# Optimization experiments

Hardware: AMD Instinct MI355X
Metric: run time of the kernel (lower is better)

Reference implementation:

```python
import jax, jax.numpy as jnp
import numpy as np

N_NODES = 65536   # sli * node = 512 * 128
N_EDGES = 524288  # avg degree 8
SLI, NODE = 512, 128
SLOPE = 0.01      # nn.LeakyReLU default negative_slope


def leaky_relu(v):
    return jnp.where(v >= 0, v, SLOPE * v)


def graph_conv(h, src, dst, W, b):
    """DGL GraphConv with norm='both': D_in^{-1/2} A D_out^{-1/2} h W + b, then LeakyReLU."""
    ones = jnp.ones(src.shape[0], dtype=h.dtype)
    out_deg = jnp.clip(jax.ops.segment_sum(ones, src, num_segments=N_NODES), 1.0)
    in_deg = jnp.clip(jax.ops.segment_sum(ones, dst, num_segments=N_NODES), 1.0)
    h = h * jax.lax.rsqrt(out_deg)[:, None]                     # src-side norm
    agg = jax.ops.segment_sum(h[src], dst, num_segments=N_NODES)  # gather + scatter-add
    agg = agg * jax.lax.rsqrt(in_deg)[:, None]                  # dst-side norm
    return leaky_relu(agg @ W + b)


def graphsage(x, src, dst, W, b):
    # x: [sli, C, node] -> [sli*node, C] -> GraphConv -> [sli, F, node]
    sli, C, node = x.shape
    h = x.transpose(0, 2, 1).reshape(-1, C)
    h = graph_conv(h, src, dst, W, b)
    return h.reshape(sli, node, -1).transpose(0, 2, 1)


def conv1x1(x, W, b):
    # pointwise Conv1d: x [S, Cin, N], W [Cout, Cin] -> [S, Cout, N]
    return jnp.einsum('scn,oc->son', x, W) + b[None, :, None]


def setup_inputs() -> dict:
    key = jax.random.key(0)
    ks = jax.random.split(key, 16)
    d = {
        'x': jax.random.normal(ks[0], (SLI, 128, NODE), dtype=jnp.float32),
        'edge_src': jax.random.randint(ks[1], (N_EDGES,), 0, N_NODES, dtype=jnp.int32),
        'edge_dst': jax.random.randint(ks[2], (N_EDGES,), 0, N_NODES, dtype=jnp.int32),
        'W_head': jax.random.normal(ks[3], (128, 128), dtype=jnp.float32) * 0.05,
        'b_head': jnp.zeros((128,), dtype=jnp.float32),
        'W_res0': jax.random.normal(ks[4], (128, 128), dtype=jnp.float32) * 0.05,
        'b_res0': jnp.zeros((128,), dtype=jnp.float32),
        'W_res1': jax.random.normal(ks[5], (128, 128), dtype=jnp.float32) * 0.05,
        'b_res1': jnp.zeros((128,), dtype=jnp.float32),
        'W_res2': jax.random.normal(ks[6], (128, 128), dtype=jnp.float32) * 0.05,
        'b_res2': jnp.zeros((128,), dtype=jnp.float32),
        'W_fusion': jax.random.normal(ks[7], (256, 512), dtype=jnp.float32) * 0.05,
        'b_fusion': jnp.zeros((256,), dtype=jnp.float32),
        'W_p1': jax.random.normal(ks[8], (256, 768), dtype=jnp.float32) * 0.05,
        'b_p1': jnp.zeros((256,), dtype=jnp.float32),
        'W_p2': jax.random.normal(ks[9], (64, 256), dtype=jnp.float32) * 0.05,
        'b_p2': jnp.zeros((64,), dtype=jnp.float32),
        'W_p3': jax.random.normal(ks[10], (2, 64), dtype=jnp.float32) * 0.05,
        'b_p3': jnp.zeros((2,), dtype=jnp.float32),
    }
    return d


def reference(x, edge_src, edge_dst, W_head, b_head, W_res0, b_res0, W_res1, b_res1,
              W_res2, b_res2, W_fusion, b_fusion, W_p1, b_p1, W_p2, b_p2, W_p3, b_p3):
    h = graphsage(x, edge_src, edge_dst, W_head, b_head)   # [S, 128, N]
    states = [h]
    for W, b in ((W_res0, b_res0), (W_res1, b_res1), (W_res2, b_res2)):
        h = graphsage(h, edge_src, edge_dst, W, b) + h     # residual
        states.append(h)
    state = jnp.concatenate(states, axis=1)                # [S, 512, N]
    fused = conv1x1(state, W_fusion, b_fusion)             # [S, 256, N]
    global_state = jnp.max(fused, axis=2, keepdims=True)   # [S, 256, 1]
    global_state = jnp.broadcast_to(global_state, (state.shape[0], 256, state.shape[2]))
    state = jnp.concatenate([global_state, state], axis=1) # [S, 768, N]
    y = leaky_relu(conv1x1(state, W_p1, b_p1))
    y = leaky_relu(conv1x1(y, W_p2, b_p2))
    return conv1x1(y, W_p3, b_p3)                          # [S, 2, N]
```

## Files before the change

### kernel.cpp

```cpp
#include <hip/hip_runtime.h>

#define NN 65536
#define NE 524288
#define SLOPE 0.01f

typedef unsigned short us;
typedef __attribute__((ext_vector_type(8))) short short8;
typedef __attribute__((ext_vector_type(4))) float f32x4;

__device__ __forceinline__ float leaky(float v) { return v >= 0.f ? v : SLOPE * v; }
__device__ __forceinline__ float b2f(us u) { return __uint_as_float(((unsigned)u) << 16); }
__device__ __forceinline__ us f2b(float f) {
  unsigned u = __float_as_uint(f);
  u += 0x7fffu + ((u >> 16) & 1u);
  return (us)(u >> 16);
}
__device__ __forceinline__ void split2(float v, us& hi, us& lo) {
  hi = f2b(v);
  lo = f2b(v - b2f(hi));
}

__device__ __forceinline__ void gload16(const void* g, void* l) {
  __builtin_amdgcn_global_load_lds(
      (const __attribute__((address_space(1))) unsigned int*)g,
      (__attribute__((address_space(3))) unsigned int*)l, 16, 0, 0);
}

__global__ void zero_ints(int* __restrict__ p, int n) {
  int i = blockIdx.x * blockDim.x + threadIdx.x;
  if (i < n) p[i] = 0;
}

__global__ void deg_count(const int* __restrict__ src, const int* __restrict__ dst,
                          int* __restrict__ cout, int* __restrict__ cin) {
  int e = blockIdx.x * blockDim.x + threadIdx.x;
  if (e < NE) {
    atomicAdd(&cout[src[e]], 1);
    atomicAdd(&cin[dst[e]], 1);
  }
}

__global__ void rs_kernel(const int* __restrict__ cout, const int* __restrict__ cin,
                          float* __restrict__ rs_out, float* __restrict__ rs_in) {
  int n = blockIdx.x * blockDim.x + threadIdx.x;
  if (n < NN) {
    rs_out[n] = rsqrtf((float)(cout[n] > 0 ? cout[n] : 1));
    rs_in[n]  = rsqrtf((float)(cin[n]  > 0 ? cin[n]  : 1));
  }
}

__global__ __launch_bounds__(1024) void scan_kernel(const int* __restrict__ cnt,
                                                    int* __restrict__ row_ptr) {
  __shared__ int part[1024];
  int t = threadIdx.x;
  int base = t * 64;
  int s = 0;
  for (int i = 0; i < 64; ++i) s += cnt[base + i];
  part[t] = s;
  __syncthreads();
  for (int d = 1; d < 1024; d <<= 1) {
    int v = (t >= d) ? part[t - d] : 0;
    __syncthreads();
    part[t] += v;
    __syncthreads();
  }
  int run = part[t] - s;
  for (int i = 0; i < 64; ++i) { row_ptr[base + i] = run; run += cnt[base + i]; }
  if (t == 1023) row_ptr[NN] = run;
}

__global__ void csr_fill(const int* __restrict__ src, const int* __restrict__ dst,
                         const int* __restrict__ row_ptr, int* __restrict__ cursor,
                         int* __restrict__ csr) {
  int e = blockIdx.x * blockDim.x + threadIdx.x;
  if (e < NE) {
    int d = dst[e];
    int pos = atomicAdd(&cursor[d], 1);
    csr[row_ptr[d] + pos] = src[e];
  }
}

__global__ __launch_bounds__(256) void transpose_x(const float* __restrict__ x,
                                                   us* __restrict__ h0h,
                                                   us* __restrict__ h0l) {
  __shared__ float tile[128][68];
  int s  = blockIdx.x >> 1;
  int vh = (blockIdx.x & 1) * 64;
  const float* xs = x + (size_t)s * 16384;
  int t = threadIdx.x;
  int v4 = t & 15, c0 = t >> 4;
  for (int p = 0; p < 8; ++p) {
    int c = c0 + p * 16;
    float4 val = *(const float4*)(xs + (size_t)c * 128 + vh + v4 * 4);
    *(float4*)&tile[c][v4 * 4] = val;
  }
  __syncthreads();
  int c4 = t & 31, v0 = t >> 5;
  for (int p = 0; p < 8; ++p) {
    int v = v0 + p * 8;
    float o[4];
    o[0] = tile[c4 * 4 + 0][v];
    o[1] = tile[c4 * 4 + 1][v];
    o[2] = tile[c4 * 4 + 2][v];
    o[3] = tile[c4 * 4 + 3][v];
    us hh[4], ll[4];
#pragma unroll
    for (int j = 0; j < 4; ++j) split2(o[j], hh[j], ll[j]);
    size_t off = (size_t)(s * 128 + vh + v) * 128 + c4 * 4;
    uint2 wh = make_uint2((unsigned)hh[0] | ((unsigned)hh[1] << 16),
                          (unsigned)hh[2] | ((unsigned)hh[3] << 16));
    uint2 wl = make_uint2((unsigned)ll[0] | ((unsigned)ll[1] << 16),
                          (unsigned)ll[2] | ((unsigned)ll[3] << 16));
    *(uint2*)(h0h + off) = wh;
    *(uint2*)(h0l + off) = wl;
  }
}

__global__ void wsplit(const float* __restrict__ src, us* __restrict__ bh,
                       us* __restrict__ bl, int N, int K, int ld, int koff) {
  int idx = blockIdx.x * 256 + threadIdx.x;
  if (idx >= N * K) return;
  int n = idx / K, k = idx - n * K;
  float v = src[(size_t)n * ld + koff + k];
  us hi, lo; split2(v, hi, lo);
  bh[idx] = hi; bl[idx] = lo;
}

__global__ void wsplit_t(const float* __restrict__ src, us* __restrict__ bh,
                         us* __restrict__ bl, int N, int K, int ld) {
  int idx = blockIdx.x * 256 + threadIdx.x;
  if (idx >= N * K) return;
  int n = idx / K, k = idx - n * K;
  float v = src[(size_t)k * ld + n];
  us hi, lo; split2(v, hi, lo);
  bh[idx] = hi; bl[idx] = lo;
}

__global__ __launch_bounds__(256) void aggregate(
    const us* __restrict__ hh, const us* __restrict__ hl, int lda,
    const int* __restrict__ row_ptr, const int* __restrict__ csr,
    const float* __restrict__ rs_out, const float* __restrict__ rs_in,
    us* __restrict__ aggh, us* __restrict__ aggl) {
  const int lane = threadIdx.x & 63;
  const int wid = threadIdx.x >> 6;
  const int half = (lane >> 5) & 1;
  const int n = blockIdx.x * 8 + wid * 2 + half;
  const bool lop = (lane & 31) >= 16;
  const int c16 = lane & 15;
  const us* base = (lop ? hl : hh) + (size_t)c16 * 8;
  const int b = row_ptr[n], e = row_ptr[n + 1];
  float a[8];
#pragma unroll
  for (int j = 0; j < 8; ++j) a[j] = 0.f;
  int i = b;
  for (; i + 4 <= e; i += 4) {
    int s0 = csr[i], s1 = csr[i + 1], s2 = csr[i + 2], s3 = csr[i + 3];
    uint4 v0 = *(const uint4*)(base + (size_t)s0 * lda);
    uint4 v1 = *(const uint4*)(base + (size_t)s1 * lda);
    uint4 v2 = *(const uint4*)(base + (size_t)s2 * lda);
    uint4 v3 = *(const uint4*)(base + (size_t)s3 * lda);
    float w0 = rs_out[s0], w1 = rs_out[s1], w2 = rs_out[s2], w3 = rs_out[s3];
    a[0] = fmaf(w0, __uint_as_float(v0.x << 16), a[0]);
    a[1] = fmaf(w0, __uint_as_float(v0.x & 0xffff0000u), a[1]);
    a[2] = fmaf(w0, __uint_as_float(v0.y << 16), a[2]);
    a[3] = fmaf(w0, __uint_as_float(v0.y & 0xffff0000u), a[3]);
    a[4] = fmaf(w0, __uint_as_float(v0.z << 16), a[4]);
    a[5] = fmaf(w0, __uint_as_float(v0.z & 0xffff0000u), a[5]);
    a[6] = fmaf(w0, __uint_as_float(v0.w << 16), a[6]);
    a[7] = fmaf(w0, __uint_as_float(v0.w & 0xffff0000u), a[7]);
    a[0] = fmaf(w1, __uint_as_float(v1.x << 16), a[0]);
    a[1] = fmaf(w1, __uint_as_float(v1.x & 0xffff0000u), a[1]);
    a[2] = fmaf(w1, __uint_as_float(v1.y << 16), a[2]);
    a[3] = fmaf(w1, __uint_as_float(v1.y & 0xffff0000u), a[3]);
    a[4] = fmaf(w1, __uint_as_float(v1.z << 16), a[4]);
    a[5] = fmaf(w1, __uint_as_float(v1.z & 0xffff0000u), a[5]);
    a[6] = fmaf(w1, __uint_as_float(v1.w << 16), a[6]);
    a[7] = fmaf(w1, __uint_as_float(v1.w & 0xffff0000u), a[7]);
    a[0] = fmaf(w2, __uint_as_float(v2.x << 16), a[0]);
    a[1] = fmaf(w2, __uint_as_float(v2.x & 0xffff0000u), a[1]);
    a[2] = fmaf(w2, __uint_as_float(v2.y << 16), a[2]);
    a[3] = fmaf(w2, __uint_as_float(v2.y & 0xffff0000u), a[3]);
    a[4] = fmaf(w2, __uint_as_float(v2.z << 16), a[4]);
    a[5] = fmaf(w2, __uint_as_float(v2.z & 0xffff0000u), a[5]);
    a[6] = fmaf(w2, __uint_as_float(v2.w << 16), a[6]);
    a[7] = fmaf(w2, __uint_as_float(v2.w & 0xffff0000u), a[7]);
    a[0] = fmaf(w3, __uint_as_float(v3.x << 16), a[0]);
    a[1] = fmaf(w3, __uint_as_float(v3.x & 0xffff0000u), a[1]);
    a[2] = fmaf(w3, __uint_as_float(v3.y << 16), a[2]);
    a[3] = fmaf(w3, __uint_as_float(v3.y & 0xffff0000u), a[3]);
    a[4] = fmaf(w3, __uint_as_float(v3.z << 16), a[4]);
    a[5] = fmaf(w3, __uint_as_float(v3.z & 0xffff0000u), a[5]);
    a[6] = fmaf(w3, __uint_as_float(v3.w << 16), a[6]);
    a[7] = fmaf(w3, __uint_as_float(v3.w & 0xffff0000u), a[7]);
  }
  for (; i < e; ++i) {
    int s0 = csr[i];
    uint4 v0 = *(const uint4*)(base + (size_t)s0 * lda);
    float w0 = rs_out[s0];
    a[0] = fmaf(w0, __uint_as_float(v0.x << 16), a[0]);
    a[1] = fmaf(w0, __uint_as_float(v0.x & 0xffff0000u), a[1]);
    a[2] = fmaf(w0, __uint_as_float(v0.y << 16), a[2]);
    a[3] = fmaf(w0, __uint_as_float(v0.y & 0xffff0000u), a[3]);
    a[4] = fmaf(w0, __uint_as_float(v0.z << 16), a[4]);
    a[5] = fmaf(w0, __uint_as_float(v0.z & 0xffff0000u), a[5]);
    a[6] = fmaf(w0, __uint_as_float(v0.w << 16), a[6]);
    a[7] = fmaf(w0, __uint_as_float(v0.w & 0xffff0000u), a[7]);
  }
#pragma unroll
  for (int j = 0; j < 8; ++j) a[j] += __shfl_xor(a[j], 16);
  const float ri = rs_in[n];
  us h8[8], l8[8];
#pragma unroll
  for (int j = 0; j < 8; ++j) split2(a[j] * ri, h8[j], l8[j]);
  size_t o = (size_t)n * 128 + (size_t)c16 * 8;
  if (!lop) {
    uint4 w = make_uint4((unsigned)h8[0] | ((unsigned)h8[1] << 16),
                         (unsigned)h8[2] | ((unsigned)h8[3] << 16),
                         (unsigned)h8[4] | ((unsigned)h8[5] << 16),
                         (unsigned)h8[6] | ((unsigned)h8[7] << 16));
    *(uint4*)(aggh + o) = w;
  } else {
    uint4 w = make_uint4((unsigned)l8[0] | ((unsigned)l8[1] << 16),
                         (unsigned)l8[2] | ((unsigned)l8[3] << 16),
                         (unsigned)l8[4] | ((unsigned)l8[5] << 16),
                         (unsigned)l8[6] | ((unsigned)l8[7] << 16));
    *(uint4*)(aggl + o) = w;
  }
}

template<int KTOT, int BN, int WM, int PH, int MODE>
__global__ __launch_bounds__(512) void mgemm8(
    const us* __restrict__ Ah, const us* __restrict__ Al, int lda,
    const us* __restrict__ Bh, const us* __restrict__ Bl,
    const float* __restrict__ bias,
    float* __restrict__ outf, us* __restrict__ outh, us* __restrict__ outl,
    int ldo, int colOff,
    const us* __restrict__ prevh, const us* __restrict__ prevl,
    const float* __restrict__ gcon) {
  constexpr int WN  = 8 / WM;
  constexpr int FM  = 16 / WM;
  constexpr int FMP = FM / PH;
  constexpr int NT  = KTOT / 32;
  constexpr int LBN = (BN == 256) ? 8 : ((BN == 128) ? 7 : 6);
  constexpr int CHT = 2048 + BN * 8;
  constexpr int LPT = CHT / 512;

  __shared__ __align__(16) us L[2][CHT * 8];

  const int t = threadIdx.x;
  const int mbase = blockIdx.x * 256;

  const us* gp[LPT];
#pragma unroll
  for (int i = 0; i < LPT; ++i) {
    int id = i * 512 + t;
    if (id < 1024) {
      int row = id & 255, kb = id >> 8;
      gp[i] = Ah + (size_t)(mbase + row) * lda + kb * 8;
    } else if (id < 2048) {
      int c = id - 1024, row = c & 255, kb = c >> 8;
      gp[i] = Al + (size_t)(mbase + row) * lda + kb * 8;
    } else if (id < 2048 + BN * 4) {
      int c = id - 2048, row = c & (BN - 1), kb = c >> LBN;
      gp[i] = Bh + (size_t)row * KTOT + kb * 8;
    } else {
      int c = id - 2048 - BN * 4, row = c & (BN - 1), kb = c >> LBN;
      gp[i] = Bl + (size_t)row * KTOT + kb * 8;
    }
  }

  const int lane = t & 63, wvi = t >> 6;
  const int wm = wvi & (WM - 1), wn = wvi / WM;
  const int l15 = lane & 15, lkb = lane >> 4;
  const int wrow = wm * (256 / WM);

  f32x4 acc[FM][4];
#pragma unroll
  for (int i = 0; i < FM; ++i)
#pragma unroll
    for (int j = 0; j < 4; ++j)
#pragma unroll
      for (int e = 0; e < 4; ++e) acc[i][j][e] = 0.f;

  auto stage = [&](us* Lb, int k0) {
#pragma unroll
    for (int i = 0; i < LPT; ++i)
      gload16(gp[i] + k0, Lb + (size_t)(i * 512 + t) * 8);
  };
  auto waitL = [&]() {
    if constexpr (LPT == 8)      asm volatile("s_waitcnt vmcnt(8)" ::: "memory");
    else if constexpr (LPT == 6) asm volatile("s_waitcnt vmcnt(6)" ::: "memory");
    else                         asm volatile("s_waitcnt vmcnt(5)" ::: "memory");
    __builtin_amdgcn_sched_barrier(0);
  };
  auto wait0 = [&]() {
    asm volatile("s_waitcnt vmcnt(0)" ::: "memory");
    __builtin_amdgcn_sched_barrier(0);
  };
  auto bar = [&]() {
    __builtin_amdgcn_s_barrier();
    __builtin_amdgcn_sched_barrier(0);
  };
  auto ktile = [&](const us* Lb) {
    short8 bh[4], bl[4];
#pragma unroll
    for (int fn = 0; fn < 4; ++fn) {
      const int bcol = wn * 64 + fn * 16 + l15;
      bh[fn] = *(const short8*)(Lb + ((size_t)(2048 + lkb * BN + bcol)) * 8);
      bl[fn] = *(const short8*)(Lb + ((size_t)(2048 + BN * 4 + lkb * BN + bcol)) * 8);
    }
#pragma unroll
    for (int p = 0; p < PH; ++p) {
      short8 ah[FMP], al[FMP];
#pragma unroll
      for (int f = 0; f < FMP; ++f) {
        const int arow = wrow + (p * FMP + f) * 16 + l15;
        ah[f] = *(const short8*)(Lb + ((size_t)(lkb * 256 + arow)) * 8);
        al[f] = *(const short8*)(Lb + ((size_t)(1024 + lkb * 256 + arow)) * 8);
      }
      __builtin_amdgcn_s_setprio(1);
#pragma unroll
      for (int f = 0; f < FMP; ++f)
#pragma unroll
        for (int fn = 0; fn < 4; ++fn)
          acc[p * FMP + f][fn] =
              __builtin_amdgcn_mfma_f32_16x16x32_bf16(ah[f], bh[fn], acc[p * FMP + f][fn], 0, 0, 0);
#pragma unroll
      for (int f = 0; f < FMP; ++f)
#pragma unroll
        for (int fn = 0; fn < 4; ++fn)
          acc[p * FMP + f][fn] =
              __builtin_amdgcn_mfma_f32_16x16x32_bf16(al[f], bh[fn], acc[p * FMP + f][fn], 0, 0, 0);
#pragma unroll
      for (int f = 0; f < FMP; ++f)
#pragma unroll
        for (int fn = 0; fn < 4; ++fn)
          acc[p * FMP + f][fn] =
              __builtin_amdgcn_mfma_f32_16x16x32_bf16(ah[f], bl[fn], acc[p * FMP + f][fn], 0, 0, 0);
      __builtin_amdgcn_s_setprio(0);
      __builtin_amdgcn_sched_barrier(0);
    }
  };

  stage(L[0], 0);
  if (NT > 1) stage(L[1], 32);
#pragma unroll 1
  for (int kt = 0; kt < NT; kt += 2) {
    waitL();
    bar();
    ktile(L[0]);
    bar();
    if (kt + 2 < NT) stage(L[0], (kt + 2) * 32);
    if (kt + 3 < NT) waitL(); else wait0();
    bar();
    ktile(L[1]);
    bar();
    if (kt + 3 < NT) stage(L[1], (kt + 3) * 32);
  }

  if constexpr (MODE == 0 || MODE == 1 || MODE == 3) {
    const float* gc = (MODE == 3) ? (gcon + (size_t)(blockIdx.x * 2 + wm) * 256) : nullptr;
#pragma unroll
    for (int fm = 0; fm < FM; ++fm)
#pragma unroll
      for (int fn = 0; fn < 4; ++fn) {
        const int col = wn * 64 + fn * 16 + l15;
        float bb = bias[col];
        if constexpr (MODE == 3) bb += gc[col];
#pragma unroll
        for (int r = 0; r < 4; ++r) {
          const int row = mbase + wrow + fm * 16 + lkb * 4 + r;
          float v = leaky(acc[fm][fn][r] + bb);
          const size_t off = (size_t)row * ldo + colOff + col;
          if constexpr (MODE == 1) v += b2f(prevh[off - 128]) + b2f(prevl[off - 128]);
          us hi, lo; split2(v, hi, lo);
          outh[off] = hi;
          outl[off] = lo;
        }
      }
  } else if constexpr (MODE == 2) {
#pragma unroll
    for (int fn = 0; fn < 4; ++fn) {
      float m = acc[0][fn][0];
#pragma unroll
      for (int fm = 0; fm < FM; ++fm)
#pragma unroll
        for (int r = 0; r < 4; ++r) m = fmaxf(m, acc[fm][fn][r]);
      m = fmaxf(m, __shfl_xor(m, 16));
      m = fmaxf(m, __shfl_xor(m, 32));
      if (lane < 16) {
        const int col = wn * 64 + fn * 16 + l15;
        outf[(size_t)(blockIdx.x * 2 + wm) * 256 + col] = m + bias[col];
      }
    }
  } else {
#pragma unroll
    for (int fm = 0; fm < FM; ++fm)
#pragma unroll
      for (int fn = 0; fn < 4; ++fn) {
        const int col = fn * 16 + l15;
        const float bb = bias[col];
#pragma unroll
        for (int r = 0; r < 4; ++r) {
          const int row = mbase + wrow + fm * 16 + lkb * 4 + r;
          outf[(size_t)row * 64 + col] = leaky(acc[fm][fn][r] + bb);
        }
      }
  }
}

__global__ void gcon_kernel(const float* __restrict__ gmax, const float* __restrict__ Wp1,
                            float* __restrict__ gcon) {
  __shared__ float g[256];
  int s = blockIdx.x, o = threadIdx.x;
  g[o] = gmax[(size_t)s * 256 + o];
  __syncthreads();
  float acc = 0.f;
  const float* wr = Wp1 + (size_t)o * 768;
#pragma unroll 8
  for (int c = 0; c < 256; ++c) acc += g[c] * wr[c];
  gcon[(size_t)s * 256 + o] = acc;
}

__global__ void p3_kernel(const float* __restrict__ y2, const float* __restrict__ W,
                          const float* __restrict__ b, float* __restrict__ out) {
  __shared__ float w0[64], w1[64];
  int t = threadIdx.x;
  if (t < 64) { w0[t] = W[t]; w1[t] = W[64 + t]; }
  __syncthreads();
  int n = blockIdx.x * 256 + t;
  const float* row = y2 + (size_t)n * 64;
  float a0 = b[0], a1 = b[1];
#pragma unroll
  for (int j = 0; j < 64; j += 4) {
    float4 v = *(const float4*)(row + j);
    a0 += v.x * w0[j] + v.y * w0[j + 1] + v.z * w0[j + 2] + v.w * w0[j + 3];
    a1 += v.x * w1[j] + v.y * w1[j + 1] + v.z * w1[j + 2] + v.w * w1[j + 3];
  }
  int s = n >> 7, vv = n & 127;
  out[((size_t)s * 2 + 0) * 128 + vv] = a0;
  out[((size_t)s * 2 + 1) * 128 + vv] = a1;
}

extern "C" void kernel_launch(void* const* d_in, const int* in_sizes, int n_in,
                              void* d_out, int out_size, void* d_ws, size_t ws_size,
                              hipStream_t stream) {
  const float* x        = (const float*)d_in[0];
  const int*   esrc     = (const int*)d_in[1];
  const int*   edst     = (const int*)d_in[2];
  const float* W_head   = (const float*)d_in[3];
  const float* b_head   = (const float*)d_in[4];
  const float* W_res[3] = {(const float*)d_in[5], (const float*)d_in[7], (const float*)d_in[9]};
  const float* b_res[3] = {(const float*)d_in[6], (const float*)d_in[8], (const float*)d_in[10]};
  const float* W_fusion = (const float*)d_in[11];
  const float* b_fusion = (const float*)d_in[12];
  const float* W_p1     = (const float*)d_in[13];
  const float* b_p1     = (const float*)d_in[14];
  const float* W_p2     = (const float*)d_in[15];
  const float* b_p2     = (const float*)d_in[16];
  const float* W_p3     = (const float*)d_in[17];
  const float* b_p3     = (const float*)d_in[18];
  float* outp = (float*)d_out;

  char* w = (char*)d_ws;
  size_t off = 0;
  auto alloc = [&](size_t bytes) { char* p = w + off; off += (bytes + 255) & ~(size_t)255; return p; };

  us* states_h = (us*)alloc((size_t)NN * 512 * 2);
  us* states_l = (us*)alloc((size_t)NN * 512 * 2);
  char* regionA = alloc((size_t)NN * 128 * 2 * 4);
  us* h0h  = (us*)regionA;
  us* h0l  = (us*)(regionA + (size_t)NN * 128 * 2);
  us* aggh = (us*)(regionA + (size_t)NN * 128 * 4);
  us* aggl = (us*)(regionA + (size_t)NN * 128 * 6);
  us* y1h  = (us*)regionA;
  us* y1l  = (us*)(regionA + (size_t)NN * 256 * 2);
  float* y2 = (float*)states_h;

  float* gmax   = (float*)alloc(512 * 256 * 4);
  float* gcon   = (float*)alloc(512 * 256 * 4);
  float* rs_out = (float*)alloc((size_t)NN * 4);
  float* rs_in  = (float*)alloc((size_t)NN * 4);
  us* cWh[4]; us* cWl[4];
  for (int l = 0; l < 4; ++l) { cWh[l] = (us*)alloc(128 * 128 * 2); cWl[l] = (us*)alloc(128 * 128 * 2); }
  us* fWh  = (us*)alloc(256 * 512 * 2);
  us* fWl  = (us*)alloc(256 * 512 * 2);
  us* p1Wh = (us*)alloc(256 * 512 * 2);
  us* p1Wl = (us*)alloc(256 * 512 * 2);
  us* p2Wh = (us*)alloc(64 * 256 * 2);
  us* p2Wl = (us*)alloc(64 * 256 * 2);
  int* cnt_out = (int*)alloc((size_t)NN * 4);
  int* cnt_in  = (int*)alloc((size_t)NN * 4);
  int* cursor  = (int*)alloc((size_t)NN * 4);
  int* row_ptr = (int*)alloc(((size_t)NN + 1) * 4);
  int* csr     = (int*)alloc((size_t)NE * 4);

  zero_ints<<<(3 * NN + 255) / 256, 256, 0, stream>>>(cnt_out, 3 * NN);
  deg_count<<<NE / 256, 256, 0, stream>>>(esrc, edst, cnt_out, cnt_in);
  rs_kernel<<<NN / 256, 256, 0, stream>>>(cnt_out, cnt_in, rs_out, rs_in);
  scan_kernel<<<1, 1024, 0, stream>>>(cnt_in, row_ptr);
  csr_fill<<<NE / 256, 256, 0, stream>>>(esrc, edst, row_ptr, cursor, csr);

  transpose_x<<<1024, 256, 0, stream>>>(x, h0h, h0l);
  const float* cW[4] = {W_head, W_res[0], W_res[1], W_res[2]};
  for (int l = 0; l < 4; ++l)
    wsplit_t<<<64, 256, 0, stream>>>(cW[l], cWh[l], cWl[l], 128, 128, 128);
  wsplit<<<512, 256, 0, stream>>>(W_fusion, fWh, fWl, 256, 512, 512, 0);
  wsplit<<<512, 256, 0, stream>>>(W_p1, p1Wh, p1Wl, 256, 512, 768, 256);
  wsplit<<<64, 256, 0, stream>>>(W_p2, p2Wh, p2Wl, 64, 256, 256, 0);

  const float* cB[4] = {b_head, b_res[0], b_res[1], b_res[2]};
  aggregate<<<NN / 8, 256, 0, stream>>>(h0h, h0l, 128, row_ptr, csr, rs_out, rs_in, aggh, aggl);
  mgemm8<128, 128, 4, 2, 0><<<256, 512, 0, stream>>>(aggh, aggl, 128, cWh[0], cWl[0], cB[0],
                                                     nullptr, states_h, states_l, 512, 0,
                                                     nullptr, nullptr, nullptr);
  for (int l = 1; l <= 3; ++l) {
    aggregate<<<NN / 8, 256, 0, stream>>>(states_h + (size_t)(l - 1) * 128,
                                          states_l + (size_t)(l - 1) * 128, 512,
                                          row_ptr, csr, rs_out, rs_in, aggh, aggl);
    mgemm8<128, 128, 4, 2, 1><<<256, 512, 0, stream>>>(aggh, aggl, 128, cWh[l], cWl[l], cB[l],
                                                       nullptr, states_h, states_l, 512, l * 128,
                                                       states_h, states_l, nullptr);
  }
  mgemm8<512, 256, 2, 4, 2><<<256, 512, 0, stream>>>(states_h, states_l, 512, fWh, fWl, b_fusion,
                                                     gmax, nullptr, nullptr, 0, 0,
                                                     nullptr, nullptr, nullptr);
  gcon_kernel<<<512, 256, 0, stream>>>(gmax, W_p1, gcon);
  mgemm8<512, 256, 2, 4, 3><<<256, 512, 0, stream>>>(states_h, states_l, 512, p1Wh, p1Wl, b_p1,
                                                     nullptr, y1h, y1l, 256, 0,
                                                     nullptr, nullptr, gcon);
  mgemm8<256, 64, 8, 2, 4><<<256, 512, 0, stream>>>(y1h, y1l, 256, p2Wh, p2Wl, b_p2,
                                                    y2, nullptr, nullptr, 0, 0,
                                                    nullptr, nullptr, nullptr);
  p3_kernel<<<NN / 256, 256, 0, stream>>>(y2, W_p3, b_p3, outp);
}
```

Before: 598.4 us.

## Add 16-wave 1024-thread GEMM kernel for conv and fusion layers

Adds mgemm16, a 1024-thread (16-wave) variant of the split-bf16 MFMA GEMM. Each wave owns a 64-row slice with 4x FN fragments, and operand staging is spread over twice as many threads. The fusion max-reduction now combines per-wave partial maxima through shared memory before writing. It is used for the graph-conv, fusion and p1 GEMMs to raise in-flight waves and latency hiding per block, at the cost of tighter register budgets per thread and an extra block-wide sync in the max epilogue. mgemm8 is trimmed to the p2-only path.

Measured after the change: 854.3 us. 1.43x slower.

```diff
diff --git a/kernel.cpp b/kernel.cpp
--- a/kernel.cpp
+++ b/kernel.cpp
@@ -228,8 +228,8 @@
   }
 }
 
-template<int KTOT, int BN, int WM, int PH, int MODE>
-__global__ __launch_bounds__(512) void mgemm8(
+template<int KTOT, int BN, int MODE>
+__global__ __launch_bounds__(1024) void mgemm16(
     const us* __restrict__ Ah, const us* __restrict__ Al, int lda,
     const us* __restrict__ Bh, const us* __restrict__ Bl,
     const float* __restrict__ bias,
@@ -237,6 +237,173 @@
     int ldo, int colOff,
     const us* __restrict__ prevh, const us* __restrict__ prevl,
     const float* __restrict__ gcon) {
+  constexpr int FN  = BN / 64;
+  constexpr int NT  = KTOT / 32;
+  constexpr int LBN = (BN == 256) ? 8 : 7;
+  constexpr int CHT = 2048 + BN * 8;
+  constexpr int LPT = CHT / 1024;
+
+  __shared__ __align__(16) us L[2][CHT * 8];
+
+  const int t = threadIdx.x;
+  const int mbase = blockIdx.x * 256;
+
+  const us* gp[LPT];
+#pragma unroll
+  for (int i = 0; i < LPT; ++i) {
+    int id = i * 1024 + t;
+    if (id < 1024) {
+      int row = id & 255, kb = id >> 8;
+      gp[i] = Ah + (size_t)(mbase + row) * lda + kb * 8;
+    } else if (id < 2048) {
+      int c = id - 1024, row = c & 255, kb = c >> 8;
+      gp[i] = Al + (size_t)(mbase + row) * lda + kb * 8;
+    } else if (id < 2048 + BN * 4) {
+      int c = id - 2048, row = c & (BN - 1), kb = c >> LBN;
+      gp[i] = Bh + (size_t)row * KTOT + kb * 8;
+    } else {
+      int c = id - 2048 - BN * 4, row = c & (BN - 1), kb = c >> LBN;
+      gp[i] = Bl + (size_t)row * KTOT + kb * 8;
+    }
+  }
+
+  const int lane = t & 63, wvi = t >> 6;
+  const int wm = wvi & 3, wn = wvi >> 2;
+  const int l15 = lane & 15, lkb = lane >> 4;
+  const int wrow = wm * 64;
+
+  f32x4 acc[4][FN];
+#pragma unroll
+  for (int i = 0; i < 4; ++i)
+#pragma unroll
+    for (int j = 0; j < FN; ++j)
+#pragma unroll
+      for (int e = 0; e < 4; ++e) acc[i][j][e] = 0.f;
+
+  auto stage = [&](us* Lb, int k0) {
+#pragma unroll
+    for (int i = 0; i < LPT; ++i)
+      gload16(gp[i] + k0, Lb + (size_t)(i * 1024 + t) * 8);
+  };
+  auto waitL = [&]() {
+    if constexpr (LPT == 4) asm volatile("s_waitcnt vmcnt(4)" ::: "memory");
+    else                    asm volatile("s_waitcnt vmcnt(3)" ::: "memory");
+    __builtin_amdgcn_sched_barrier(0);
+  };
+  auto wait0 = [&]() {
+    asm volatile("s_waitcnt vmcnt(0)" ::: "memory");
+    __builtin_amdgcn_sched_barrier(0);
+  };
+  auto bar = [&]() {
+    __builtin_amdgcn_s_barrier();
+    __builtin_amdgcn_sched_barrier(0);
+  };
+  auto ktile = [&](const us* Lb) {
+    short8 bh[FN], bl[FN];
+#pragma unroll
+    for (int fn = 0; fn < FN; ++fn) {
+      const int bcol = wn * (FN * 16) + fn * 16 + l15;
+      bh[fn] = *(const short8*)(Lb + ((size_t)(2048 + lkb * BN + bcol)) * 8);
+      bl[fn] = *(const short8*)(Lb + ((size_t)(2048 + BN * 4 + lkb * BN + bcol)) * 8);
+    }
+#pragma unroll
+    for (int p = 0; p < 2; ++p) {
+      short8 ah[2], al[2];
+#pragma unroll
+      for (int f = 0; f < 2; ++f) {
+        const int arow = wrow + (p * 2 + f) * 16 + l15;
+        ah[f] = *(const short8*)(Lb + ((size_t)(lkb * 256 + arow)) * 8);
+        al[f] = *(const short8*)(Lb + ((size_t)(1024 + lkb * 256 + arow)) * 8);
+      }
+      __builtin_amdgcn_s_setprio(1);
+#pragma unroll
+      for (int f = 0; f < 2; ++f)
+#pragma unroll
+        for (int fn = 0; fn < FN; ++fn)
+          acc[p * 2 + f][fn] =
+              __builtin_amdgcn_mfma_f32_16x16x32_bf16(ah[f], bh[fn], acc[p * 2 + f][fn], 0, 0, 0);
+#pragma unroll
+      for (int f = 0; f < 2; ++f)
+#pragma unroll
+        for (int fn = 0; fn < FN; ++fn)
+          acc[p * 2 + f][fn] =
+              __builtin_amdgcn_mfma_f32_16x16x32_bf16(al[f], bh[fn], acc[p * 2 + f][fn], 0, 0, 0);
+#pragma unroll
+      for (int f = 0; f < 2; ++f)
+#pragma unroll
+        for (int fn = 0; fn < FN; ++fn)
+          acc[p * 2 + f][fn] =
+              __builtin_amdgcn_mfma_f32_16x16x32_bf16(ah[f], bl[fn], acc[p * 2 + f][fn], 0, 0, 0);
+      __builtin_amdgcn_s_setprio(0);
+      __builtin_amdgcn_sched_barrier(0);
+    }
+  };
+
+  stage(L[0], 0);
+  if (NT > 1) stage(L[1], 32);
+#pragma unroll 1
+  for (int kt = 0; kt < NT; kt += 2) {
+    waitL();
+    bar();
+    ktile(L[0]);
+    bar();
+    if (kt + 2 < NT) stage(L[0], (kt + 2) * 32);
+    if (kt + 3 < NT) waitL(); else wait0();
+    bar();
+    ktile(L[1]);
+    bar();
+    if (kt + 3 < NT) stage(L[1], (kt + 3) * 32);
+  }
+
+  if constexpr (MODE == 0 || MODE == 1 || MODE == 3) {
+    const float* gc = (MODE == 3) ? (gcon + (size_t)(blockIdx.x * 2 + (wm >> 1)) * 256) : nullptr;
+#pragma unroll
+    for (int fm = 0; fm < 4; ++fm)
+#pragma unroll
+      for (int fn = 0; fn < FN; ++fn) {
+        const int col = wn * (FN * 16) + fn * 16 + l15;
+        float bb = bias[col];
+        if constexpr (MODE == 3) bb += gc[col];
+#pragma unroll
+        for (int r = 0; r < 4; ++r) {
+          const int row = mbase + wrow + fm * 16 + lkb * 4 + r;
+          float v = leaky(acc[fm][fn][r] + bb);
+          const size_t off = (size_t)row * ldo + colOff + col;
+          if constexpr (MODE == 1) v += b2f(prevh[off - 128]) + b2f(prevl[off - 128]);
+          us hi, lo; split2(v, hi, lo);
+          outh[off] = hi;
+          outl[off] = lo;
+        }
+      }
+  } else if constexpr (MODE == 2) {
+    __shared__ float red[4][256];
+#pragma unroll
+    for (int fn = 0; fn < FN; ++fn) {
+      float m = acc[0][fn][0];
+#pragma unroll
+      for (int fm = 0; fm < 4; ++fm)
+#pragma unroll
+        for (int r = 0; r < 4; ++r) m = fmaxf(m, acc[fm][fn][r]);
+      m = fmaxf(m, __shfl_xor(m, 16));
+      m = fmaxf(m, __shfl_xor(m, 32));
+      if (lane < 16) red[wm][wn * (FN * 16) + fn * 16 + l15] = m;
+    }
+    __syncthreads();
+    if (t < 512) {
+      int s = t >> 8, col = t & 255;
+      float m = fmaxf(red[2 * s][col], red[2 * s + 1][col]);
+      outf[(size_t)(blockIdx.x * 2 + s) * 256 + col] = m + bias[col];
+    }
+  }
+}
+
+template<int KTOT, int BN, int WM, int PH, int MODE>
+__global__ __launch_bounds__(512) void mgemm8(
+    const us* __restrict__ Ah, const us* __restrict__ Al, int lda,
+    const us* __restrict__ Bh, const us* __restrict__ Bl,
+    const float* __restrict__ bias,
+    float* __restrict__ outf, us* __restrict__ outh, us* __restrict__ outl,
+    int ldo, int colOff) {
   constexpr int WN  = 8 / WM;
   constexpr int FM  = 16 / WM;
   constexpr int FMP = FM / PH;
@@ -358,55 +525,18 @@
     if (kt + 3 < NT) stage(L[1], (kt + 3) * 32);
   }
 
-  if constexpr (MODE == 0 || MODE == 1 || MODE == 3) {
-    const float* gc = (MODE == 3) ? (gcon + (size_t)(blockIdx.x * 2 + wm) * 256) : nullptr;
-#pragma unroll
-    for (int fm = 0; fm < FM; ++fm)
-#pragma unroll
-      for (int fn = 0; fn < 4; ++fn) {
-        const int col = wn * 64 + fn * 16 + l15;
-        float bb = bias[col];
-        if constexpr (MODE == 3) bb += gc[col];
-#pragma unroll
-        for (int r = 0; r < 4; ++r) {
-          const int row = mbase + wrow + fm * 16 + lkb * 4 + r;
-          float v = leaky(acc[fm][fn][r] + bb);
-          const size_t off = (size_t)row * ldo + colOff + col;
-          if constexpr (MODE == 1) v += b2f(prevh[off - 128]) + b2f(prevl[off - 128]);
-          us hi, lo; split2(v, hi, lo);
-          outh[off] = hi;
-          outl[off] = lo;
-        }
+#pragma unroll
+  for (int fm = 0; fm < FM; ++fm)
+#pragma unroll
+    for (int fn = 0; fn < 4; ++fn) {
+      const int col = fn * 16 + l15;
+      const float bb = bias[col];
+#pragma unroll
+      for (int r = 0; r < 4; ++r) {
+        const int row = mbase + wrow + fm * 16 + lkb * 4 + r;
+        outf[(size_t)row * 64 + col] = leaky(acc[fm][fn][r] + bb);
       }
-  } else if constexpr (MODE == 2) {
-#pragma unroll
-    for (int fn = 0; fn < 4; ++fn) {
-      float m = acc[0][fn][0];
-#pragma unroll
-      for (int fm = 0; fm < FM; ++fm)
-#pragma unroll
-        for (int r = 0; r < 4; ++r) m = fmaxf(m, acc[fm][fn][r]);
-      m = fmaxf(m, __shfl_xor(m, 16));
-      m = fmaxf(m, __shfl_xor(m, 32));
-      if (lane < 16) {
-        const int col = wn * 64 + fn * 16 + l15;
-        outf[(size_t)(blockIdx.x * 2 + wm) * 256 + col] = m + bias[col];
-      }
-    }
-  } else {
-#pragma unroll
-    for (int fm = 0; fm < FM; ++fm)
-#pragma unroll
-      for (int fn = 0; fn < 4; ++fn) {
-        const int col = fn * 16 + l15;
-        const float bb = bias[col];
-#pragma unroll
-        for (int r = 0; r < 4; ++r) {
-          const int row = mbase + wrow + fm * 16 + lkb * 4 + r;
-          outf[(size_t)row * 64 + col] = leaky(acc[fm][fn][r] + bb);
-        }
-      }
-  }
+    }
 }
 
 __global__ void gcon_kernel(const float* __restrict__ gmax, const float* __restrict__ Wp1,
@@ -511,26 +641,25 @@
 
   const float* cB[4] = {b_head, b_res[0], b_res[1], b_res[2]};
   aggregate<<<NN / 8, 256, 0, stream>>>(h0h, h0l, 128, row_ptr, csr, rs_out, rs_in, aggh, aggl);
-  mgemm8<128, 128, 4, 2, 0><<<256, 512, 0, stream>>>(aggh, aggl, 128, cWh[0], cWl[0], cB[0],
-                                                     nullptr, states_h, states_l, 512, 0,
-                                                     nullptr, nullptr, nullptr);
+  mgemm16<128, 128, 0><<<256, 1024, 0, stream>>>(aggh, aggl, 128, cWh[0], cWl[0], cB[0],
+                                                 nullptr, states_h, states_l, 512, 0,
+                                                 nullptr, nullptr, nullptr);
   for (int l = 1; l <= 3; ++l) {
     aggregate<<<NN / 8, 256, 0, stream>>>(states_h + (size_t)(l - 1) * 128,
                                           states_l + (size_t)(l - 1) * 128, 512,
                                           row_ptr, csr, rs_out, rs_in, aggh, aggl);
-    mgemm8<128, 128, 4, 2, 1><<<256, 512, 0, stream>>>(aggh, aggl, 128, cWh[l], cWl[l], cB[l],
-                                                       nullptr, states_h, states_l, 512, l * 128,
-                                                       states_h, states_l, nullptr);
-  }
-  mgemm8<512, 256, 2, 4, 2><<<256, 512, 0, stream>>>(states_h, states_l, 512, fWh, fWl, b_fusion,
-                                                     gmax, nullptr, nullptr, 0, 0,
-                                                     nullptr, nullptr, nullptr);
+    mgemm16<128, 128, 1><<<256, 1024, 0, stream>>>(aggh, aggl, 128, cWh[l], cWl[l], cB[l],
+                                                   nullptr, states_h, states_l, 512, l * 128,
+                                                   states_h, states_l, nullptr);
+  }
+  mgemm16<512, 256, 2><<<256, 1024, 0, stream>>>(states_h, states_l, 512, fWh, fWl, b_fusion,
+                                                 gmax, nullptr, nullptr, 0, 0,
+                                                 nullptr, nullptr, nullptr);
   gcon_kernel<<<512, 256, 0, stream>>>(gmax, W_p1, gcon);
-  mgemm8<512, 256, 2, 4, 3><<<256, 512, 0, stream>>>(states_h, states_l, 512, p1Wh, p1Wl, b_p1,
-                                                     nullptr, y1h, y1l, 256, 0,
-                                                     nullptr, nullptr, gcon);
+  mgemm16<512, 256, 3><<<256, 1024, 0, stream>>>(states_h, states_l, 512, p1Wh, p1Wl, b_p1,
+                                                 nullptr, y1h, y1l, 256, 0,
+                                                 nullptr, nullptr, gcon);
   mgemm8<256, 64, 8, 2, 4><<<256, 512, 0, stream>>>(y1h, y1l, 256, p2Wh, p2Wl, b_p2,
-                                                    y2, nullptr, nullptr, 0, 0,
-                                                    nullptr, nullptr, nullptr);
+                                                    y2, nullptr, nullptr, 0, 0);
   p3_kernel<<<NN / 256, 256, 0, stream>>>(y2, W_p3, b_p3, outp);
 }
```
